# Performance work log

Measured on AMD Instinct MI355X. Metric: run time of the kernel, lower is better.

## Reference

```python
import jax, jax.numpy as jnp
import numpy as np

B = 65536
OBS_DIM = 85          # input_shape
FEAT = 8              # dim_entity_feature
NL = 5                # dim_landmarks
NT = 10               # dim_total
INF = 64              # in_features == out_features
HID = 64              # rnn_hidden_dim
NACT = 5              # n_actions
ALPHA = 0.01


def _leaky(x):
    return jnp.where(x > 0, x, ALPHA * x)


def setup_inputs() -> dict:
    key = jax.random.key(0)
    ks = jax.random.split(key, 26)
    s = 0.1
    d = {
        'obs': jax.random.normal(ks[0], (B, OBS_DIM), jnp.float32),
        'hidden_state': jax.random.normal(ks[1], (B, HID), jnp.float32),
        # entity input projections (input_layer_0/1/2), stored [in, out]
        'w_in0': jax.random.normal(ks[2], (FEAT, INF), jnp.float32) * s,
        'b_in0': jax.random.normal(ks[3], (INF,), jnp.float32) * s,
        'w_in1': jax.random.normal(ks[4], (FEAT, INF), jnp.float32) * s,
        'b_in1': jax.random.normal(ks[5], (INF,), jnp.float32) * s,
        'w_in2': jax.random.normal(ks[6], (FEAT, INF), jnp.float32) * s,
        'b_in2': jax.random.normal(ks[7], (INF,), jnp.float32) * s,
        # GAT params
        'W': jax.random.normal(ks[8], (INF, INF), jnp.float32) * s,
        'a': jax.random.normal(ks[9], (2 * INF, 1), jnp.float32) * s,
        # output MLP on attention rows (dim_soft = 2*dim_nearby = 10)
        'w_o1': jax.random.normal(ks[10], (2 * NL, 32), jnp.float32) * s,
        'b_o1': jax.random.normal(ks[11], (32,), jnp.float32) * s,
        'w_o2': jax.random.normal(ks[12], (32, 16), jnp.float32) * s,
        'b_o2': jax.random.normal(ks[13], (16,), jnp.float32) * s,
        'w_o3': jax.random.normal(ks[14], (16, 1), jnp.float32) * s,
        'b_o3': jax.random.normal(ks[15], (1,), jnp.float32) * s,
        # fc1 takes obs (85) concat atom_plug (5) -> 90
        'w_fc1': jax.random.normal(ks[16], (OBS_DIM + NL, HID), jnp.float32) * s,
        'b_fc1': jax.random.normal(ks[17], (HID,), jnp.float32) * s,
        # GRUCell, torch layout: [3H, in]
        'w_ih': jax.random.normal(ks[18], (3 * HID, HID), jnp.float32) * s,
        'w_hh': jax.random.normal(ks[19], (3 * HID, HID), jnp.float32) * s,
        'b_ih': jax.random.normal(ks[20], (3 * HID,), jnp.float32) * s,
        'b_hh': jax.random.normal(ks[21], (3 * HID,), jnp.float32) * s,
        'w_fc2': jax.random.normal(ks[22], (HID, NACT), jnp.float32) * s,
        'b_fc2': jax.random.normal(ks[23], (NACT,), jnp.float32) * s,
    }
    return d


def reference(obs, hidden_state, w_in0, b_in0, w_in1, b_in1, w_in2, b_in2,
              W, a, w_o1, b_o1, w_o2, b_o2, w_o3, b_o3,
              w_fc1, b_fc1, w_ih, w_hh, b_ih, b_hh, w_fc2, b_fc2):
    # data_preprocess: drop last dim_nearby cols, rotate first 4 to back, reshape to entities
    o = obs[:, :OBS_DIM - NL]                               # [B, 80]
    obs_in = jnp.concatenate([o[:, 4:], o[:, :4]], axis=-1).reshape(-1, NT, FEAT)  # [B,10,8]

    h0 = _leaky(obs_in @ w_in0 + b_in0)                     # [B,10,64]
    h1 = _leaky(obs_in @ w_in1 + b_in1)
    h2 = _leaky(obs_in @ w_in2 + b_in2)
    h_mix = jnp.concatenate([h0[:, :NL], h1[:, NL:NT - 1], h2[:, NT - 1:NT]], axis=1)  # [B,10,64]

    Wh = h_mix @ W                                          # [B,10,64]
    Wh1 = Wh @ a[:INF]                                      # [B,10,1]
    Wh2 = Wh @ a[INF:]                                      # [B,10,1]
    e = _leaky(Wh1 + jnp.swapaxes(Wh2, 1, 2))               # [B,10,10]

    att0 = jax.nn.softmax(e[:, :NL, NL:], axis=-1)          # [B,5,5]
    att1 = jnp.swapaxes(jax.nn.softmax(e[:, NL:, :NL], axis=-1), 1, 2)  # [B,5,5]
    attention = jnp.concatenate([att0, att1], axis=-1)      # [B,5,10]

    hp = _leaky(attention @ w_o1 + b_o1)
    hp = _leaky(hp @ w_o2 + b_o2)
    hp = _leaky(hp @ w_o3 + b_o3)[..., 0]                   # [B,5]
    obs_out = jax.nn.softmax(hp, axis=-1)                   # [B,5]

    obs_comb = jnp.concatenate([obs, obs_out], axis=-1)     # [B,90]
    x = jax.nn.relu(obs_comb @ w_fc1 + b_fc1)               # [B,64]

    h_in = hidden_state.reshape(-1, HID)
    gi = x @ w_ih.T + b_ih                                  # [B,192]
    gh = h_in @ w_hh.T + b_hh
    r = jax.nn.sigmoid(gi[:, :HID] + gh[:, :HID])
    z = jax.nn.sigmoid(gi[:, HID:2 * HID] + gh[:, HID:2 * HID])
    n = jnp.tanh(gi[:, 2 * HID:] + r * gh[:, 2 * HID:])
    h = (1.0 - z) * n + z * h_in                            # [B,64]

    q = h @ w_fc2 + b_fc2                                   # [B,5]
    return (q, h)
```

## Files before the change

kernel.cpp:

```cpp
#include <hip/hip_runtime.h>
#include <math.h>

namespace {

typedef __bf16 bf16x8 __attribute__((ext_vector_type(8)));
typedef float  f32x4  __attribute__((ext_vector_type(4)));
typedef float  f32x2  __attribute__((ext_vector_type(2)));

constexpr int B_      = 65536;
constexpr int OBS_DIM_= 85;
constexpr int NL_     = 5;
constexpr int NT_     = 10;
constexpr int HID_    = 64;
constexpr int NACT_   = 5;
constexpr float ALPHA_= 0.01f;

__device__ __forceinline__ float leaky(float x)    { return x > 0.0f ? x : ALPHA_ * x; }
__device__ __forceinline__ float sigmoidf(float x) { return 1.0f / (1.0f + __expf(-x)); }
__device__ __forceinline__ float tanh_fast(float x){ return 1.0f - 2.0f / (__expf(2.0f * x) + 1.0f); }

__global__ void prep_kernel(const float* __restrict__ W, const float* __restrict__ a,
                            const float* __restrict__ w_ih, const float* __restrict__ w_hh,
                            const float* __restrict__ w_fc1, void* __restrict__ ws) {
  float* Wa   = (float*)ws;
  __bf16* ih  = (__bf16*)((char*)ws + 512);
  __bf16* hh  = ih + 192 * 64;
  __bf16* f1t = hh + 192 * 64;
  const int tid = blockIdx.x * 256 + threadIdx.x;
  if (blockIdx.x == 0 && threadIdx.x < 64) {
    const int i = threadIdx.x;
    float s1 = 0.0f, s2 = 0.0f;
    #pragma unroll
    for (int j = 0; j < 64; ++j) {
      float w = W[i * 64 + j];
      s1 += w * a[j];
      s2 += w * a[64 + j];
    }
    Wa[i] = s1;
    Wa[64 + i] = s2;
  }
  const int stride = gridDim.x * 256;
  for (int i = tid; i < 192 * 64; i += stride) {
    ih[i] = (__bf16)w_ih[i];
    hh[i] = (__bf16)w_hh[i];
  }
  for (int i = tid; i < 64 * 96; i += stride) {
    int n = i / 96, k = i - 96 * n;
    f1t[i] = (__bf16)(k < 90 ? w_fc1[k * 64 + n] : 0.0f);
  }
}


__global__ __launch_bounds__(256) void front_kernel(
    const float* __restrict__ obs,
    const float* __restrict__ w_in0, const float* __restrict__ b_in0,
    const float* __restrict__ w_in1, const float* __restrict__ b_in1,
    const float* __restrict__ w_in2, const float* __restrict__ b_in2,
    const float* __restrict__ w_o1, const float* __restrict__ b_o1,
    const float* __restrict__ w_o2, const float* __restrict__ b_o2,
    const float* __restrict__ w_o3, const float* __restrict__ b_o3,
    const float* __restrict__ Wa,
    float* __restrict__ out5) {

  __shared__ __align__(16) float s_obs[8][84];
  __shared__ float s_wh1[8][12], s_wh2[8][12];
  __shared__ float s_colm[8][6], s_cols[8][6];
  __shared__ float s_att[8][5][11];
  __shared__ float s_h1[8][5][33];
  __shared__ float s_h2[8][5][17];
  __shared__ float s_hp[8][6];

  const int tid    = threadIdx.x;
  const int wv     = tid >> 6;
  const int lane   = tid & 63;
  const int lane32 = lane & 31;
  const int rloc   = tid >> 5;
  const long gr0   = (long)blockIdx.x * 8;

  {
    const float* src = obs + (gr0 + 2 * wv) * OBS_DIM_;
    #pragma unroll
    for (int c0 = 0; c0 < 3; ++c0) {
      int it = c0 * 64 + lane;
      if (it < 160) {
        int r = (it >= 80) ? 1 : 0;
        int c = it - 80 * r;
        s_obs[2 * wv + r][c] = src[r * OBS_DIM_ + c];
      }
    }
  }

  const int half = lane32 >> 4;
  const int l16  = lane32 & 15;
  const int u0   = l16 * 4;
  const float* orow = s_obs[rloc];

  const f32x4 wa1 = *(const f32x4*)&Wa[u0];
  const f32x4 wa2 = *(const f32x4*)&Wa[64 + u0];

  const float* wcA = half ? w_in1 : w_in0;
  const float* bcA = half ? b_in1 : b_in0;
  f32x4 wA[8];
  #pragma unroll
  for (int f = 0; f < 8; ++f) wA[f] = *(const f32x4*)&wcA[f * 64 + u0];
  f32x4 bA = *(const f32x4*)&bcA[u0];

  #pragma unroll
  for (int p = 0; p < 5; ++p) {
    if (p == 4 && half) {
      #pragma unroll
      for (int f = 0; f < 8; ++f) wA[f] = *(const f32x4*)&w_in2[f * 64 + u0];
      bA = *(const f32x4*)&b_in2[u0];
    }
    const int t  = p + (half ? 5 : 0);
    int ia = t * 8 + 4;
    int ib = t * 8 + 8;
    if (ib >= 80) ib = 0;
    f32x4 oa = *(const f32x4*)&orow[ia];
    f32x4 ob = *(const f32x4*)&orow[ib];
    f32x4 z = bA;
    #pragma unroll
    for (int f = 0; f < 4; ++f) {
      z[0] += oa[f] * wA[f][0]; z[1] += oa[f] * wA[f][1];
      z[2] += oa[f] * wA[f][2]; z[3] += oa[f] * wA[f][3];
    }
    #pragma unroll
    for (int f = 4; f < 8; ++f) {
      z[0] += ob[f - 4] * wA[f][0]; z[1] += ob[f - 4] * wA[f][1];
      z[2] += ob[f - 4] * wA[f][2]; z[3] += ob[f - 4] * wA[f][3];
    }
    float h0 = leaky(z[0]), h1 = leaky(z[1]), h2 = leaky(z[2]), h3 = leaky(z[3]);
    float p1t = h0 * wa1[0] + h1 * wa1[1] + h2 * wa1[2] + h3 * wa1[3];
    float p2t = h0 * wa2[0] + h1 * wa2[1] + h2 * wa2[2] + h3 * wa2[3];
    p1t += __shfl_xor(p1t, 1, 64);  p2t += __shfl_xor(p2t, 1, 64);
    p1t += __shfl_xor(p1t, 2, 64);  p2t += __shfl_xor(p2t, 2, 64);
    p1t += __shfl_xor(p1t, 4, 64);  p2t += __shfl_xor(p2t, 4, 64);
    p1t += __shfl_xor(p1t, 8, 64);  p2t += __shfl_xor(p2t, 8, 64);
    if (l16 == 0) { s_wh1[rloc][t] = p1t; s_wh2[rloc][t] = p2t; }
  }

  if (lane32 >= 5 && lane32 < 10) {
    const int jj = lane32 - 5;
    float w1v = s_wh1[rloc][NL_ + jj];
    float ev[NL_], m = -1e30f;
    #pragma unroll
    for (int k = 0; k < NL_; ++k) { ev[k] = leaky(w1v + s_wh2[rloc][k]); m = fmaxf(m, ev[k]); }
    float s = 0.0f;
    #pragma unroll
    for (int k = 0; k < NL_; ++k) s += __expf(ev[k] - m);
    s_colm[rloc][jj] = m;
    s_cols[rloc][jj] = s;
  }

  if (lane32 < NL_) {
    const int r = lane32;
    const float wh1_r = s_wh1[rloc][r];
    const float wh2_r = s_wh2[rloc][r];
    float ev[NL_], m = -1e30f;
    #pragma unroll
    for (int j = 0; j < NL_; ++j) { ev[j] = leaky(wh1_r + s_wh2[rloc][NL_ + j]); m = fmaxf(m, ev[j]); }
    float a0[NL_], s = 0.0f;
    #pragma unroll
    for (int j = 0; j < NL_; ++j) { a0[j] = __expf(ev[j] - m); s += a0[j]; }
    float inv = 1.0f / s;
    #pragma unroll
    for (int j = 0; j < NL_; ++j) s_att[rloc][r][j] = a0[j] * inv;
    #pragma unroll
    for (int jj = 0; jj < NL_; ++jj) {
      float e = leaky(s_wh1[rloc][NL_ + jj] + wh2_r);
      s_att[rloc][r][NL_ + jj] = __expf(e - s_colm[rloc][jj]) / s_cols[rloc][jj];
    }
  }

  #pragma unroll
  for (int r5 = 0; r5 < NL_; ++r5) {
    float z = b_o1[lane32];
    #pragma unroll
    for (int k = 0; k < NT_; ++k) z += s_att[rloc][r5][k] * w_o1[k * 32 + lane32];
    s_h1[rloc][r5][lane32] = leaky(z);
  }

  #pragma unroll
  for (int b0 = 0; b0 < 3; ++b0) {
    int it = b0 * 32 + lane32;
    if (it < 80) {
      int r5 = it >> 4, c = it & 15;
      float z = b_o2[c];
      #pragma unroll
      for (int k = 0; k < 32; ++k) z += s_h1[rloc][r5][k] * w_o2[k * 16 + c];
      s_h2[rloc][r5][c] = leaky(z);
    }
  }

  if (lane32 < NL_) {
    float z3 = b_o3[0];
    #pragma unroll
    for (int k = 0; k < 16; ++k) z3 += s_h2[rloc][lane32][k] * w_o3[k];
    float hp_own = leaky(z3);
    s_hp[rloc][lane32] = hp_own;
    float m5 = -1e30f;
    #pragma unroll
    for (int j = 0; j < NL_; ++j) m5 = fmaxf(m5, s_hp[rloc][j]);
    float ssum = 0.0f;
    #pragma unroll
    for (int j = 0; j < NL_; ++j) ssum += __expf(s_hp[rloc][j] - m5);
    out5[(gr0 + rloc) * NL_ + lane32] = __expf(hp_own - m5) / ssum;
  }
}

constexpr int ROWS_ = 64;
constexpr int SOB_  = 104;
constexpr int SXH_  = 72;

__global__ __launch_bounds__(256) void gemm_kernel(
    const float* __restrict__ obs, const float* __restrict__ hidden,
    const float* __restrict__ b_fc1,
    const float* __restrict__ b_ih, const float* __restrict__ b_hh,
    const float* __restrict__ w_fc2, const float* __restrict__ b_fc2,
    const void* __restrict__ wsv,
    float* q5,
    float* __restrict__ h_out) {

  __shared__ __align__(16) __bf16 A_obs[ROWS_ * SOB_];
  __shared__ __align__(16) __bf16 A_x[ROWS_ * SXH_];

  const int tid  = threadIdx.x;
  const int wv   = tid >> 6;
  const int lane = tid & 63;
  const int l    = lane & 15;
  const int quad = lane >> 4;
  const int r0   = wv * 16;
  const long gr0 = (long)blockIdx.x * ROWS_;

  const __bf16* Wih = (const __bf16*)((const char*)wsv + 512);
  const __bf16* Whh = Wih + 192 * 64;
  const __bf16* Wf1 = Whh + 192 * 64;

  {
    const float* src = obs + (gr0 + r0) * OBS_DIM_;
    #pragma unroll
    for (int k = 0; k < 6; ++k) {
      int idx = lane + 64 * k;
      if (idx < 340) {
        f32x4 v = *(const f32x4*)&src[idx * 4];
        #pragma unroll
        for (int e = 0; e < 4; ++e) {
          int fe = idx * 4 + e;
          int rr = fe / 85, cc = fe - 85 * rr;
          A_obs[(r0 + rr) * SOB_ + cc] = (__bf16)v[e];
        }
      }
    }
    const float* o5 = q5 + (gr0 + r0) * NL_;
    for (int it = lane; it < 16 * NL_; it += 64) {
      int rr = it / NL_; int cc = it - rr * NL_;
      A_obs[(r0 + rr) * SOB_ + 85 + cc] = (__bf16)o5[it];
    }
    for (int it = lane; it < 16 * 6; it += 64) {
      int rr = it / 6; int cc = it - rr * 6;
      A_obs[(r0 + rr) * SOB_ + 90 + cc] = (__bf16)0.0f;
    }
  }

  const f32x4 zero4 = {0.0f, 0.0f, 0.0f, 0.0f};

  bf16x8 ah[2];
  {
    const float* hrow_g = hidden + (gr0 + r0 + l) * HID_;
    #pragma unroll
    for (int ks = 0; ks < 2; ++ks) {
      f32x4 va = *(const f32x4*)&hrow_g[ks * 32 + quad * 8];
      f32x4 vb = *(const f32x4*)&hrow_g[ks * 32 + quad * 8 + 4];
      bf16x8 t;
      t[0] = (__bf16)va[0]; t[1] = (__bf16)va[1]; t[2] = (__bf16)va[2]; t[3] = (__bf16)va[3];
      t[4] = (__bf16)vb[0]; t[5] = (__bf16)vb[1]; t[6] = (__bf16)vb[2]; t[7] = (__bf16)vb[3];
      ah[ks] = t;
    }
  }

  f32x4 cx[4];
  #pragma unroll
  for (int nt = 0; nt < 4; ++nt) cx[nt] = zero4;
  #pragma unroll
  for (int ks = 0; ks < 3; ++ks) {
    bf16x8 af = *(const bf16x8*)&A_obs[(r0 + l) * SOB_ + ks * 32 + quad * 8];
    #pragma unroll
    for (int nt = 0; nt < 4; ++nt) {
      bf16x8 bf = *(const bf16x8*)&Wf1[(nt * 16 + l) * 96 + ks * 32 + quad * 8];
      cx[nt] = __builtin_amdgcn_mfma_f32_16x16x32_bf16(af, bf, cx[nt], 0, 0, 0);
    }
  }
  #pragma unroll
  for (int nt = 0; nt < 4; ++nt) {
    float bias = b_fc1[nt * 16 + l];
    #pragma unroll
    for (int rg = 0; rg < 4; ++rg) {
      float xv = fmaxf(cx[nt][rg] + bias, 0.0f);
      A_x[(r0 + quad * 4 + rg) * SXH_ + nt * 16 + l] = (__bf16)xv;
    }
  }

  bf16x8 ax[2];
  #pragma unroll
  for (int ks = 0; ks < 2; ++ks)
    ax[ks] = *(const bf16x8*)&A_x[(r0 + l) * SXH_ + ks * 32 + quad * 8];

  f32x4 crz[8], cni[4], cnh[4];
  #pragma unroll
  for (int nt = 0; nt < 8; ++nt) crz[nt] = zero4;
  #pragma unroll
  for (int nt = 0; nt < 4; ++nt) { cni[nt] = zero4; cnh[nt] = zero4; }
  #pragma unroll
  for (int nt = 0; nt < 8; ++nt) {
    #pragma unroll
    for (int ks = 0; ks < 2; ++ks) {
      bf16x8 bi = *(const bf16x8*)&Wih[(nt * 16 + l) * 64 + ks * 32 + quad * 8];
      crz[nt] = __builtin_amdgcn_mfma_f32_16x16x32_bf16(ax[ks], bi, crz[nt], 0, 0, 0);
      bf16x8 bh = *(const bf16x8*)&Whh[(nt * 16 + l) * 64 + ks * 32 + quad * 8];
      crz[nt] = __builtin_amdgcn_mfma_f32_16x16x32_bf16(ah[ks], bh, crz[nt], 0, 0, 0);
    }
  }
  #pragma unroll
  for (int nt = 0; nt < 4; ++nt) {
    #pragma unroll
    for (int ks = 0; ks < 2; ++ks) {
      bf16x8 bi = *(const bf16x8*)&Wih[(128 + nt * 16 + l) * 64 + ks * 32 + quad * 8];
      cni[nt] = __builtin_amdgcn_mfma_f32_16x16x32_bf16(ax[ks], bi, cni[nt], 0, 0, 0);
      bf16x8 bh = *(const bf16x8*)&Whh[(128 + nt * 16 + l) * 64 + ks * 32 + quad * 8];
      cnh[nt] = __builtin_amdgcn_mfma_f32_16x16x32_bf16(ah[ks], bh, cnh[nt], 0, 0, 0);
    }
  }

  const long grow = gr0 + r0 + quad * 4;
  float qp[4][NACT_];
  #pragma unroll
  for (int rg = 0; rg < 4; ++rg)
    #pragma unroll
    for (int c = 0; c < NACT_; ++c) qp[rg][c] = 0.0f;

  #pragma unroll
  for (int t = 0; t < 4; ++t) {
    const int ur = t * 16 + l;
    float br  = b_ih[ur] + b_hh[ur];
    float bz  = b_ih[64 + ur] + b_hh[64 + ur];
    float bin = b_ih[128 + ur], bhn = b_hh[128 + ur];
    float w0 = w_fc2[ur * 5 + 0], w1 = w_fc2[ur * 5 + 1], w2 = w_fc2[ur * 5 + 2];
    float w3 = w_fc2[ur * 5 + 3], w4 = w_fc2[ur * 5 + 4];
    #pragma unroll
    for (int rg = 0; rg < 4; ++rg) {
      float rr = sigmoidf(crz[t][rg] + br);
      float zz = sigmoidf(crz[4 + t][rg] + bz);
      float nn = tanh_fast(cni[t][rg] + bin + rr * (cnh[t][rg] + bhn));
      float hold = hidden[(grow + rg) * HID_ + ur];
      float hn = (1.0f - zz) * nn + zz * hold;
      h_out[(grow + rg) * HID_ + ur] = hn;
      qp[rg][0] += hn * w0;
      qp[rg][1] += hn * w1;
      qp[rg][2] += hn * w2;
      qp[rg][3] += hn * w3;
      qp[rg][4] += hn * w4;
    }
  }
  #pragma unroll
  for (int m = 1; m < 16; m <<= 1) {
    #pragma unroll
    for (int rg = 0; rg < 4; ++rg)
      #pragma unroll
      for (int c = 0; c < NACT_; ++c) qp[rg][c] += __shfl_xor(qp[rg][c], m, 64);
  }
  if (l < NACT_) {
    #pragma unroll
    for (int rg = 0; rg < 4; ++rg) {
      float qv = qp[rg][0];
      if (l == 1) qv = qp[rg][1];
      if (l == 2) qv = qp[rg][2];
      if (l == 3) qv = qp[rg][3];
      if (l == 4) qv = qp[rg][4];
      q5[(grow + rg) * NACT_ + l] = qv + b_fc2[l];
    }
  }
}

}

extern "C" void kernel_launch(void* const* d_in, const int* in_sizes, int n_in,
                              void* d_out, int out_size, void* d_ws, size_t ws_size,
                              hipStream_t stream) {
  const float* obs    = (const float*)d_in[0];
  const float* hidden = (const float*)d_in[1];
  const float* w_in0  = (const float*)d_in[2];
  const float* b_in0  = (const float*)d_in[3];
  const float* w_in1  = (const float*)d_in[4];
  const float* b_in1  = (const float*)d_in[5];
  const float* w_in2  = (const float*)d_in[6];
  const float* b_in2  = (const float*)d_in[7];
  const float* W      = (const float*)d_in[8];
  const float* a      = (const float*)d_in[9];
  const float* w_o1   = (const float*)d_in[10];
  const float* b_o1   = (const float*)d_in[11];
  const float* w_o2   = (const float*)d_in[12];
  const float* b_o2   = (const float*)d_in[13];
  const float* w_o3   = (const float*)d_in[14];
  const float* b_o3   = (const float*)d_in[15];
  const float* w_fc1  = (const float*)d_in[16];
  const float* b_fc1  = (const float*)d_in[17];
  const float* w_ih   = (const float*)d_in[18];
  const float* w_hh   = (const float*)d_in[19];
  const float* b_ih   = (const float*)d_in[20];
  const float* b_hh   = (const float*)d_in[21];
  const float* w_fc2  = (const float*)d_in[22];
  const float* b_fc2  = (const float*)d_in[23];

  float* q_out = (float*)d_out;
  float* h_out = q_out + (long)B_ * NACT_;
  const float* Wa = (const float*)d_ws;

  prep_kernel<<<48, 256, 0, stream>>>(W, a, w_ih, w_hh, w_fc1, d_ws);
  front_kernel<<<B_ / 8, 256, 0, stream>>>(
      obs, w_in0, b_in0, w_in1, b_in1, w_in2, b_in2,
      w_o1, b_o1, w_o2, b_o2, w_o3, b_o3, Wa, q_out);
  gemm_kernel<<<B_ / ROWS_, 256, 0, stream>>>(
      obs, hidden, b_fc1, b_ih, b_hh, w_fc2, b_fc2, d_ws, q_out, h_out);
}
```

Measured before the change: 237.0 us.

## Process 16 rows per block in front kernel with 16-lane row groups

The front kernel now assigns 16 lanes per batch row instead of 32, so each block handles 16 rows and the grid is halved. Each row group walks all ten entities sequentially, reloading the projection weights for the second and third entity types. The output MLP layers cache their weight columns in registers and read shared-memory activations as vectors, and leaky ReLU becomes a branchless fmin/fma. This aims to cut idle lanes and per-row overhead, at the cost of more register pressure and longer serial loops per lane group.

```diff
diff --git a/kernel.cpp b/kernel.cpp
--- a/kernel.cpp
+++ b/kernel.cpp
@@ -15,7 +15,7 @@
 constexpr int NACT_   = 5;
 constexpr float ALPHA_= 0.01f;
 
-__device__ __forceinline__ float leaky(float x)    { return x > 0.0f ? x : ALPHA_ * x; }
+__device__ __forceinline__ float leaky(float x)    { return fmaf(fminf(x, 0.0f), ALPHA_ - 1.0f, x); }
 __device__ __forceinline__ float sigmoidf(float x) { return 1.0f / (1.0f + __expf(-x)); }
 __device__ __forceinline__ float tanh_fast(float x){ return 1.0f - 2.0f / (__expf(2.0f * x) + 1.0f); }
 
@@ -62,58 +62,54 @@
     const float* __restrict__ Wa,
     float* __restrict__ out5) {
 
-  __shared__ __align__(16) float s_obs[8][84];
-  __shared__ float s_wh1[8][12], s_wh2[8][12];
-  __shared__ float s_colm[8][6], s_cols[8][6];
-  __shared__ float s_att[8][5][11];
-  __shared__ float s_h1[8][5][33];
-  __shared__ float s_h2[8][5][17];
-  __shared__ float s_hp[8][6];
-
-  const int tid    = threadIdx.x;
-  const int wv     = tid >> 6;
-  const int lane   = tid & 63;
-  const int lane32 = lane & 31;
-  const int rloc   = tid >> 5;
-  const long gr0   = (long)blockIdx.x * 8;
+  __shared__ __align__(16) float s_obs[16][84];
+  __shared__ float s_wh1[16][12], s_wh2[16][12];
+  __shared__ float s_colm[16][6], s_cols[16][6];
+  __shared__ __align__(16) float s_att[16][5][12];
+  __shared__ __align__(16) float s_h1[16][5][36];
+  __shared__ __align__(16) float s_h2[16][5][20];
+  __shared__ float s_hp[16][6];
+
+  const int tid  = threadIdx.x;
+  const int wv   = tid >> 6;
+  const int lane = tid & 63;
+  const int l16  = lane & 15;
+  const int rloc = tid >> 4;
+  const long gr0 = (long)blockIdx.x * 16;
 
   {
-    const float* src = obs + (gr0 + 2 * wv) * OBS_DIM_;
-    #pragma unroll
-    for (int c0 = 0; c0 < 3; ++c0) {
+    const float* src = obs + (gr0 + wv * 4) * OBS_DIM_;
+    #pragma unroll
+    for (int c0 = 0; c0 < 5; ++c0) {
       int it = c0 * 64 + lane;
-      if (it < 160) {
-        int r = (it >= 80) ? 1 : 0;
-        int c = it - 80 * r;
-        s_obs[2 * wv + r][c] = src[r * OBS_DIM_ + c];
-      }
-    }
-  }
-
-  const int half = lane32 >> 4;
-  const int l16  = lane32 & 15;
-  const int u0   = l16 * 4;
+      int r = it / 80, c = it - 80 * r;
+      s_obs[wv * 4 + r][c] = src[r * OBS_DIM_ + c];
+    }
+  }
+
+  const int u0 = l16 * 4;
   const float* orow = s_obs[rloc];
-
   const f32x4 wa1 = *(const f32x4*)&Wa[u0];
   const f32x4 wa2 = *(const f32x4*)&Wa[64 + u0];
 
-  const float* wcA = half ? w_in1 : w_in0;
-  const float* bcA = half ? b_in1 : b_in0;
   f32x4 wA[8];
   #pragma unroll
-  for (int f = 0; f < 8; ++f) wA[f] = *(const f32x4*)&wcA[f * 64 + u0];
-  f32x4 bA = *(const f32x4*)&bcA[u0];
-
-  #pragma unroll
-  for (int p = 0; p < 5; ++p) {
-    if (p == 4 && half) {
+  for (int f = 0; f < 8; ++f) wA[f] = *(const f32x4*)&w_in0[f * 64 + u0];
+  f32x4 bA = *(const f32x4*)&b_in0[u0];
+
+  #pragma unroll
+  for (int t = 0; t < NT_; ++t) {
+    if (t == 5) {
+      #pragma unroll
+      for (int f = 0; f < 8; ++f) wA[f] = *(const f32x4*)&w_in1[f * 64 + u0];
+      bA = *(const f32x4*)&b_in1[u0];
+    }
+    if (t == 9) {
       #pragma unroll
       for (int f = 0; f < 8; ++f) wA[f] = *(const f32x4*)&w_in2[f * 64 + u0];
       bA = *(const f32x4*)&b_in2[u0];
     }
-    const int t  = p + (half ? 5 : 0);
-    int ia = t * 8 + 4;
+    const int ia = t * 8 + 4;
     int ib = t * 8 + 8;
     if (ib >= 80) ib = 0;
     f32x4 oa = *(const f32x4*)&orow[ia];
@@ -139,8 +135,8 @@
     if (l16 == 0) { s_wh1[rloc][t] = p1t; s_wh2[rloc][t] = p2t; }
   }
 
-  if (lane32 >= 5 && lane32 < 10) {
-    const int jj = lane32 - 5;
+  if (l16 >= 5 && l16 < 10) {
+    const int jj = l16 - 5;
     float w1v = s_wh1[rloc][NL_ + jj];
     float ev[NL_], m = -1e30f;
     #pragma unroll
@@ -152,8 +148,8 @@
     s_cols[rloc][jj] = s;
   }
 
-  if (lane32 < NL_) {
-    const int r = lane32;
+  if (l16 < NL_) {
+    const int r = l16;
     const float wh1_r = s_wh1[rloc][r];
     const float wh2_r = s_wh2[rloc][r];
     float ev[NL_], m = -1e30f;
@@ -172,39 +168,59 @@
     }
   }
 
-  #pragma unroll
-  for (int r5 = 0; r5 < NL_; ++r5) {
-    float z = b_o1[lane32];
-    #pragma unroll
-    for (int k = 0; k < NT_; ++k) z += s_att[rloc][r5][k] * w_o1[k * 32 + lane32];
-    s_h1[rloc][r5][lane32] = leaky(z);
-  }
-
-  #pragma unroll
-  for (int b0 = 0; b0 < 3; ++b0) {
-    int it = b0 * 32 + lane32;
-    if (it < 80) {
-      int r5 = it >> 4, c = it & 15;
-      float z = b_o2[c];
+  {
+    f32x2 w1c[NT_];
+    #pragma unroll
+    for (int k = 0; k < NT_; ++k) w1c[k] = *(const f32x2*)&w_o1[k * 32 + l16 * 2];
+    const f32x2 b1 = *(const f32x2*)&b_o1[l16 * 2];
+    #pragma unroll
+    for (int r5 = 0; r5 < NL_; ++r5) {
+      float za = b1[0], zb = b1[1];
       #pragma unroll
-      for (int k = 0; k < 32; ++k) z += s_h1[rloc][r5][k] * w_o2[k * 16 + c];
-      s_h2[rloc][r5][c] = leaky(z);
-    }
-  }
-
-  if (lane32 < NL_) {
+      for (int k2 = 0; k2 < 5; ++k2) {
+        f32x2 at = *(const f32x2*)&s_att[rloc][r5][k2 * 2];
+        za += at[0] * w1c[2 * k2][0] + at[1] * w1c[2 * k2 + 1][0];
+        zb += at[0] * w1c[2 * k2][1] + at[1] * w1c[2 * k2 + 1][1];
+      }
+      *(f32x2*)&s_h1[rloc][r5][l16 * 2] = f32x2{leaky(za), leaky(zb)};
+    }
+  }
+
+  {
+    float w2c[32];
+    #pragma unroll
+    for (int k = 0; k < 32; ++k) w2c[k] = w_o2[k * 16 + l16];
+    const float b2 = b_o2[l16];
+    #pragma unroll
+    for (int r5 = 0; r5 < NL_; ++r5) {
+      float z = b2;
+      #pragma unroll
+      for (int k4 = 0; k4 < 8; ++k4) {
+        f32x4 hv = *(const f32x4*)&s_h1[rloc][r5][k4 * 4];
+        z += hv[0] * w2c[4 * k4] + hv[1] * w2c[4 * k4 + 1]
+           + hv[2] * w2c[4 * k4 + 2] + hv[3] * w2c[4 * k4 + 3];
+      }
+      s_h2[rloc][r5][l16] = leaky(z);
+    }
+  }
+
+  if (l16 < NL_) {
     float z3 = b_o3[0];
     #pragma unroll
-    for (int k = 0; k < 16; ++k) z3 += s_h2[rloc][lane32][k] * w_o3[k];
+    for (int k4 = 0; k4 < 4; ++k4) {
+      f32x4 hv = *(const f32x4*)&s_h2[rloc][l16][k4 * 4];
+      z3 += hv[0] * w_o3[4 * k4] + hv[1] * w_o3[4 * k4 + 1]
+          + hv[2] * w_o3[4 * k4 + 2] + hv[3] * w_o3[4 * k4 + 3];
+    }
     float hp_own = leaky(z3);
-    s_hp[rloc][lane32] = hp_own;
+    s_hp[rloc][l16] = hp_own;
     float m5 = -1e30f;
     #pragma unroll
     for (int j = 0; j < NL_; ++j) m5 = fmaxf(m5, s_hp[rloc][j]);
     float ssum = 0.0f;
     #pragma unroll
     for (int j = 0; j < NL_; ++j) ssum += __expf(s_hp[rloc][j] - m5);
-    out5[(gr0 + rloc) * NL_ + lane32] = __expf(hp_own - m5) / ssum;
+    out5[(gr0 + rloc) * NL_ + l16] = __expf(hp_own - m5) / ssum;
   }
 }
 
@@ -416,7 +432,7 @@
   const float* Wa = (const float*)d_ws;
 
   prep_kernel<<<48, 256, 0, stream>>>(W, a, w_ih, w_hh, w_fc1, d_ws);
-  front_kernel<<<B_ / 8, 256, 0, stream>>>(
+  front_kernel<<<B_ / 16, 256, 0, stream>>>(
       obs, w_in0, b_in0, w_in1, b_in1, w_in2, b_in2,
       w_o1, b_o1, w_o2, b_o2, w_o3, b_o3, Wa, q_out);
   gemm_kernel<<<B_ / ROWS_, 256, 0, stream>>>(
```

Measured after the change: 206.2 us. 13.0% less time.
